# Kernel tuning notes

Hardware: AMD Instinct MI355X
Metric: run time of the kernel (lower is better)

Reference implementation:

```python
import jax, jax.numpy as jnp
import numpy as np

E, H, KVH, D = 2048, 16, 4, 128      # embed_dim, heads, kv heads, head_dim
HG, R, SYM, VAN = 12, 32, 4, 4       # graph heads, rel_rank, sym heads, vanilla heads
BASE = 10000
EPS = 1e-6


def _rms_norm(x, w):
    # RMSNorm over last dim (head_dim)
    return x * jax.lax.rsqrt(jnp.mean(x * x, axis=-1, keepdims=True) + EPS) * w


def _rotate_half(x):
    x1, x2 = jnp.split(x, 2, axis=-1)
    return jnp.concatenate([-x2, x1], axis=-1)


def _rope(q, k):
    # q, k: [B, H, S, D]
    S = q.shape[2]
    inv_freq = 1.0 / (BASE ** (jnp.arange(0, D, 2, dtype=jnp.float32) / D))
    t = jnp.arange(S, dtype=jnp.float32)
    freqs = jnp.outer(t, inv_freq)                       # [S, D/2]
    emb = jnp.concatenate([freqs, freqs], axis=-1)       # [S, D]
    cos = jnp.cos(emb)[None, None].astype(q.dtype)
    sin = jnp.sin(emb)[None, None].astype(q.dtype)
    return q * cos + _rotate_half(q) * sin, k * cos + _rotate_half(k) * sin


def setup_inputs() -> dict:
    key = jax.random.key(0)
    ks = jax.random.split(key, 9)
    B, S = 1, 2048
    std = 0.02
    return {
        'x': jax.random.normal(ks[0], (B, S, E), jnp.float32),
        'Wq': jax.random.normal(ks[1], (E, E), jnp.float32) * std,
        'Wk': jax.random.normal(ks[2], (KVH * D, E), jnp.float32) * std,
        'Wv': jax.random.normal(ks[3], (KVH * D, E), jnp.float32) * std,
        'Wo': jax.random.normal(ks[4], (E, E), jnp.float32) * std,
        'q_norm_w': jnp.ones((D,), jnp.float32),
        'k_norm_w': jnp.ones((D,), jnp.float32),
        'Wrq': jax.random.normal(ks[5], (HG * R, E), jnp.float32) * 0.01,
        'Wrk': jax.random.normal(ks[6], (HG * R, E), jnp.float32) * 0.01,
        'graph_scale': jax.random.normal(ks[7], (HG,), jnp.float32) * 0.1,
    }


def reference(x, Wq, Wk, Wv, Wo, q_norm_w, k_norm_w, Wrq, Wrk, graph_scale):
    B, S, _ = x.shape
    # projections -> [B, heads, S, D]
    q = (x @ Wq.T).reshape(B, S, H, D).transpose(0, 2, 1, 3)
    k = (x @ Wk.T).reshape(B, S, KVH, D).transpose(0, 2, 1, 3)
    v = (x @ Wv.T).reshape(B, S, KVH, D).transpose(0, 2, 1, 3)
    # QK-norm then RoPE
    q = _rms_norm(q, q_norm_w)
    k = _rms_norm(k, k_norm_w)
    q, k = _rope(q, k)
    # GQA: repeat kv heads
    rep = H // KVH
    k = jnp.repeat(k, rep, axis=1)
    v = jnp.repeat(v, rep, axis=1)
    # low-rank graph bias: [B, HG, S, S]
    Rq = (x @ Wrq.T).reshape(B, S, HG, R).transpose(0, 2, 1, 3)
    Rk = (x @ Wrk.T).reshape(B, S, HG, R).transpose(0, 2, 1, 3)
    bias = jnp.einsum('bhsr,bhtr->bhst', Rq, Rk)
    sym = bias[:, :SYM]
    sym = (sym + sym.transpose(0, 1, 3, 2)) * 0.5
    bias = jnp.concatenate([sym, bias[:, SYM:]], axis=1)
    bias = bias * graph_scale[None, :, None, None]
    # vanilla heads (last VAN heads) get zero bias
    bias = jnp.concatenate([bias, jnp.zeros((B, VAN, S, S), bias.dtype)], axis=1)
    # attention with causal mask
    scale = 1.0 / np.sqrt(D).astype(np.float32)
    scores = jnp.einsum('bhsd,bhtd->bhst', q, k) * scale + bias
    causal = jnp.tril(jnp.ones((S, S), bool))
    scores = jnp.where(causal[None, None], scores, jnp.finfo(scores.dtype).min)
    attn = jax.nn.softmax(scores, axis=-1)
    out = jnp.einsum('bhst,bhtd->bhsd', attn, v)
    out = out.transpose(0, 2, 1, 3).reshape(B, S, E)
    return out @ Wo.T
```

## Files before the change

kernel.cpp:

```cpp
#include <hip/hip_runtime.h>
#include <hip/hip_bf16.h>

typedef __attribute__((ext_vector_type(8))) short short8;
typedef __attribute__((ext_vector_type(4))) float f32x4;

__device__ __forceinline__ f32x4 mfma16(short8 a, short8 b, f32x4 c) {
  return __builtin_amdgcn_mfma_f32_16x16x32_bf16(a, b, c, 0, 0, 0);
}

__device__ __forceinline__ void gload_lds16(const void* g, void* l) {
  __builtin_amdgcn_global_load_lds(
      (const __attribute__((address_space(1))) void*)g,
      (__attribute__((address_space(3))) void*)l, 16, 0, 0);
}

struct __align__(8) bh4 { __hip_bfloat16 a, b, c, d; };
struct CastSeg { const float* src; __hip_bfloat16* dst; int n4; };
struct CastArgs { CastSeg seg[7]; int tot4; };

__global__ __launch_bounds__(256) void cast_all(CastArgs a) {
  int i = blockIdx.x * 256 + threadIdx.x;
  const int stride = gridDim.x * 256;
  for (; i < a.tot4; i += stride) {
    int j = i, s = 0;
    while (j >= a.seg[s].n4) { j -= a.seg[s].n4; ++s; }
    float4 v = ((const float4*)a.seg[s].src)[j];
    bh4 o{__float2bfloat16(v.x), __float2bfloat16(v.y),
          __float2bfloat16(v.z), __float2bfloat16(v.w)};
    ((bh4*)a.seg[s].dst)[j] = o;
  }
}

__global__ __launch_bounds__(256) void gemm_bt(const __hip_bfloat16* __restrict__ A,
                                               const __hip_bfloat16* __restrict__ B,
                                               float* __restrict__ C,
                                               int N, int K) {
  __shared__ __align__(16) __hip_bfloat16 As[128][32];
  __shared__ __align__(16) __hip_bfloat16 Bs[128][32];

  const int tid = threadIdx.x;
  const int lane = tid & 63, wv = tid >> 6;
  const int wm = (wv >> 1) * 64, wn = (wv & 1) * 64;
  const int l15 = lane & 15, g = lane >> 4;
  const int mb = blockIdx.y * 128, nb = blockIdx.x * 128;

  const int srow = wv * 32 + (lane >> 2);
  const int scol = (lane & 3) * 8;
  const __hip_bfloat16* Ap = A + (size_t)(mb + srow) * K + scol;
  const __hip_bfloat16* Bp = B + (size_t)(nb + srow) * K + scol;
  __hip_bfloat16* lA0 = &As[wv * 32][0];
  __hip_bfloat16* lA1 = &As[wv * 32 + 16][0];
  __hip_bfloat16* lB0 = &Bs[wv * 32][0];
  __hip_bfloat16* lB1 = &Bs[wv * 32 + 16][0];

  const f32x4 zf = {0.f, 0.f, 0.f, 0.f};
  f32x4 acc[4][4];
#pragma unroll
  for (int m = 0; m < 4; ++m)
#pragma unroll
    for (int n = 0; n < 4; ++n) acc[m][n] = zf;

  for (int k0 = 0; k0 < K; k0 += 32) {
    __syncthreads();
    gload_lds16(Ap + k0, lA0);
    gload_lds16(Ap + (size_t)16 * K + k0, lA1);
    gload_lds16(Bp + k0, lB0);
    gload_lds16(Bp + (size_t)16 * K + k0, lB1);
    __syncthreads();
    short8 af[4], bf[4];
#pragma unroll
    for (int m = 0; m < 4; ++m) af[m] = *(const short8*)&As[wm + m * 16 + l15][g * 8];
#pragma unroll
    for (int n = 0; n < 4; ++n) bf[n] = *(const short8*)&Bs[wn + n * 16 + l15][g * 8];
#pragma unroll
    for (int m = 0; m < 4; ++m)
#pragma unroll
      for (int n = 0; n < 4; ++n) acc[m][n] = mfma16(af[m], bf[n], acc[m][n]);
  }

#pragma unroll
  for (int m = 0; m < 4; ++m)
#pragma unroll
    for (int n = 0; n < 4; ++n)
#pragma unroll
      for (int r = 0; r < 4; ++r)
        C[(size_t)(mb + wm + m * 16 + g * 4 + r) * N + (nb + wn + n * 16 + l15)] =
            acc[m][n][r];
}

__global__ __launch_bounds__(256) void postproc(const float* __restrict__ C1,
                                                const float* __restrict__ qw,
                                                const float* __restrict__ kw,
                                                __hip_bfloat16* __restrict__ qn,
                                                __hip_bfloat16* __restrict__ kn,
                                                __hip_bfloat16* __restrict__ vt,
                                                __hip_bfloat16* __restrict__ rq,
                                                __hip_bfloat16* __restrict__ rk) {
  constexpr int S = 2048;
  const int s = blockIdx.x;
  const int tid = threadIdx.x;
  const int lane = tid & 63;
  const int wv = tid >> 6;
  const float* row = C1 + (size_t)s * 3840;

  const float f = exp2f(-(float)lane * (13.287712379549449f / 64.0f));
  const float ang = (float)s * f;
  float sn, cs;
  sincosf(ang, &sn, &cs);

  for (int hr = wv; hr < 20; hr += 4) {
    const float* base;
    __hip_bfloat16* dst;
    const float* nw;
    float oscale;
    if (hr < 16) {
      base = row + hr * 128;
      dst = qn + ((size_t)hr * S + s) * 128;
      nw = qw;
      oscale = 0.08838834764831845f;
    } else {
      const int h4 = hr - 16;
      base = row + 2048 + h4 * 128;
      dst = kn + ((size_t)h4 * S + s) * 128;
      nw = kw;
      oscale = 1.0f;
    }
    const float x1 = base[lane], x2 = base[lane + 64];
    float ss = x1 * x1 + x2 * x2;
#pragma unroll
    for (int mk = 1; mk < 64; mk <<= 1) ss += __shfl_xor(ss, mk);
    const float rms = rsqrtf(ss * (1.0f / 128.0f) + 1e-6f);
    const float x1n = x1 * rms * nw[lane];
    const float x2n = x2 * rms * nw[lane + 64];
    dst[lane]      = __float2bfloat16((x1n * cs - x2n * sn) * oscale);
    dst[lane + 64] = __float2bfloat16((x2n * cs + x1n * sn) * oscale);
  }
  for (int i = tid; i < 512; i += 256) {
    const int h4 = i >> 7, d = i & 127;
    vt[((size_t)h4 * 128 + d) * S + s] = __float2bfloat16(row[2560 + i]);
  }
  for (int i = tid; i < 768; i += 256) {
    if (i < 384) {
      rq[((size_t)(i >> 5) * S + s) * 32 + (i & 31)] = __float2bfloat16(row[3072 + i]);
    } else {
      const int j = i - 384;
      rk[((size_t)(j >> 5) * S + s) * 32 + (j & 31)] = __float2bfloat16(row[3072 + i]);
    }
  }
}

__global__ __launch_bounds__(256) void attn_kernel(const __hip_bfloat16* __restrict__ qn,
                                                   const __hip_bfloat16* __restrict__ kn,
                                                   const __hip_bfloat16* __restrict__ vt,
                                                   const __hip_bfloat16* __restrict__ rq,
                                                   const __hip_bfloat16* __restrict__ rk,
                                                   const float* __restrict__ gsc,
                                                   __hip_bfloat16* __restrict__ ao) {
  constexpr int S = 2048;
  constexpr float L2E = 1.4426950408889634f;
  const int h = blockIdx.x & 15;
  const int qb = 31 - (blockIdx.x >> 4);
  const int tid = threadIdx.x;
  const int lane = tid & 63;
  const int wv = tid >> 6;
  const int qs = qb * 64 + wv * 16;
  const int l15 = lane & 15, g = lane >> 4;
  const int h4 = h >> 2;
  const bool has_bias = (h < 12);
  const bool symh = (h < 4);
  const float gs = has_bias ? gsc[h] : 0.0f;
  const f32x4 zf = {0.f, 0.f, 0.f, 0.f};

  __shared__ __align__(16) char KsRaw[2][16384];
  __shared__ __align__(16) char VsRaw[2][16384];
  __shared__ __align__(16) __hip_bfloat16 p_lds[4][16][72];

  const int sxk = ((tid >> 4) & 7) << 4;
  const int sxv = ((tid >> 3) & 7) << 4;
  const int k_wr = (tid * 16) ^ sxk;
  const int v_wr = (tid * 16) ^ sxv;
  const int kx = (l15 & 7) << 4;

  short8 qf[4];
  {
    const __hip_bfloat16* qrow = qn + ((size_t)h * S + qs + l15) * 128 + g * 8;
#pragma unroll
    for (int kc = 0; kc < 4; ++kc) qf[kc] = *(const short8*)(qrow + kc * 32);
  }
  short8 rqA = {}, rkA = {};
  if (has_bias) rqA = *(const short8*)(rq + ((size_t)h * S + qs + l15) * 32 + g * 8);
  if (symh)     rkA = *(const short8*)(rk + ((size_t)h * S + qs + l15) * 32 + g * 8);

  float l_r[4] = {0.f, 0.f, 0.f, 0.f};
  f32x4 acc[8];
#pragma unroll
  for (int fb = 0; fb < 8; ++fb) acc[fb] = zf;

  const int nt = qb + 1;

  short8 kreg[4], vreg[4];
#pragma unroll
  for (int c = 0; c < 4; ++c) {
    kreg[c] = *(const short8*)(kn + ((size_t)(h4 * S + c * 16 + (tid >> 4))) * 128 + (tid & 15) * 8);
    vreg[c] = *(const short8*)(vt + ((size_t)(h4 * 128 + c * 32 + (tid >> 3))) * S + (tid & 7) * 8);
  }
#pragma unroll
  for (int c = 0; c < 4; ++c) {
    *(short8*)(&KsRaw[0][c * 4096 + k_wr]) = kreg[c];
    *(short8*)(&VsRaw[0][c * 4096 + v_wr]) = vreg[c];
  }
  if (nt > 1) {
#pragma unroll
    for (int c = 0; c < 4; ++c) {
      kreg[c] = *(const short8*)(kn + ((size_t)(h4 * S + 64 + c * 16 + (tid >> 4))) * 128 + (tid & 15) * 8);
      vreg[c] = *(const short8*)(vt + ((size_t)(h4 * 128 + c * 32 + (tid >> 3))) * S + 64 + (tid & 7) * 8);
    }
  }
  short8 rkB[4], rqB[4];
  if (has_bias) {
#pragma unroll
    for (int tf = 0; tf < 4; ++tf)
      rkB[tf] = *(const short8*)(rk + ((size_t)h * S + tf * 16 + l15) * 32 + g * 8);
    if (symh) {
#pragma unroll
      for (int tf = 0; tf < 4; ++tf)
        rqB[tf] = *(const short8*)(rq + ((size_t)h * S + tf * 16 + l15) * 32 + g * 8);
    }
  }
  __syncthreads();

  for (int t = 0; t < nt; ++t) {
    const int tbase = t * 64;
    const char* ksb = &KsRaw[t & 1][0];
    const char* vsb = &VsRaw[t & 1][0];

    f32x4 bias4[4];
    if (has_bias) {
#pragma unroll
      for (int tf = 0; tf < 4; ++tf) bias4[tf] = mfma16(rqA, rkB[tf], zf);
      if (symh) {
#pragma unroll
        for (int tf = 0; tf < 4; ++tf) {
          f32x4 b2 = mfma16(rkA, rqB[tf], zf);
#pragma unroll
          for (int r = 0; r < 4; ++r) bias4[tf][r] = 0.5f * (bias4[tf][r] + b2[r]);
        }
      }
      if (t + 1 < nt) {
        const int tb2 = tbase + 64;
#pragma unroll
        for (int tf = 0; tf < 4; ++tf)
          rkB[tf] = *(const short8*)(rk + ((size_t)h * S + tb2 + tf * 16 + l15) * 32 + g * 8);
        if (symh) {
#pragma unroll
          for (int tf = 0; tf < 4; ++tf)
            rqB[tf] = *(const short8*)(rq + ((size_t)h * S + tb2 + tf * 16 + l15) * 32 + g * 8);
        }
      }
    }

    f32x4 sc[4];
#pragma unroll
    for (int tf = 0; tf < 4; ++tf) {
      f32x4 s4 = zf;
#pragma unroll
      for (int kc = 0; kc < 4; ++kc) {
        short8 kf = *(const short8*)(ksb + ((((tf * 16 + l15) << 8) + (kc << 6) + (g << 4)) ^ kx));
        s4 = mfma16(qf[kc], kf, s4);
      }
#pragma unroll
      for (int r = 0; r < 4; ++r) {
        float sv = s4[r];
        if (has_bias) sv += gs * bias4[tf][r];
        if (tbase + tf * 16 + l15 > qs + g * 4 + r) sv = -1e30f;
        sc[tf][r] = sv;
      }
    }

#pragma unroll
    for (int tf = 0; tf < 4; ++tf)
#pragma unroll
      for (int r = 0; r < 4; ++r) {
        const float p = exp2f(sc[tf][r] * L2E);
        sc[tf][r] = p;
        l_r[r] += p;
      }

#pragma unroll
    for (int tf = 0; tf < 4; ++tf)
#pragma unroll
      for (int r = 0; r < 4; ++r)
        p_lds[wv][g * 4 + r][tf * 16 + l15] = __float2bfloat16(sc[tf][r]);
    const short8 pa0 = *(const short8*)((const char*)&p_lds[wv][l15][0] + g * 16);
    const short8 pa1 = *(const short8*)((const char*)&p_lds[wv][l15][32] + g * 16);

#pragma unroll
    for (int fb = 0; fb < 8; ++fb) {
      short8 v0 = *(const short8*)(vsb + ((((fb * 16 + l15) << 7) + (g << 4)) ^ kx));
      short8 v1 = *(const short8*)(vsb + ((((fb * 16 + l15) << 7) + 64 + (g << 4)) ^ kx));
      acc[fb] = mfma16(pa0, v0, acc[fb]);
      acc[fb] = mfma16(pa1, v1, acc[fb]);
    }

    if (t + 1 < nt) {
      char* ksw = &KsRaw[(t + 1) & 1][0];
      char* vsw = &VsRaw[(t + 1) & 1][0];
#pragma unroll
      for (int c = 0; c < 4; ++c) {
        *(short8*)(ksw + c * 4096 + k_wr) = kreg[c];
        *(short8*)(vsw + c * 4096 + v_wr) = vreg[c];
      }
      if (t + 2 < nt) {
        const int tb3 = tbase + 128;
#pragma unroll
        for (int c = 0; c < 4; ++c) {
          kreg[c] = *(const short8*)(kn + ((size_t)(h4 * S + tb3 + c * 16 + (tid >> 4))) * 128 + (tid & 15) * 8);
          vreg[c] = *(const short8*)(vt + ((size_t)(h4 * 128 + c * 32 + (tid >> 3))) * S + tb3 + (tid & 7) * 8);
        }
      }
      __syncthreads();
    }
  }

#pragma unroll
  for (int r = 0; r < 4; ++r) {
    float lv = l_r[r];
    lv += __shfl_xor(lv, 1);
    lv += __shfl_xor(lv, 2);
    lv += __shfl_xor(lv, 4);
    lv += __shfl_xor(lv, 8);
    l_r[r] = lv;
  }

#pragma unroll
  for (int fb = 0; fb < 8; ++fb)
#pragma unroll
    for (int r = 0; r < 4; ++r) {
      const int srow = qs + g * 4 + r;
      ao[(size_t)srow * 2048 + h * 128 + fb * 16 + l15] =
          __float2bfloat16(acc[fb][r] / l_r[r]);
    }
}

extern "C" void kernel_launch(void* const* d_in, const int* in_sizes, int n_in,
                              void* d_out, int out_size, void* d_ws, size_t ws_size,
                              hipStream_t stream) {
  (void)in_sizes; (void)n_in; (void)out_size; (void)ws_size;
  constexpr int S = 2048, E = 2048;

  const float* x   = (const float*)d_in[0];
  const float* Wq  = (const float*)d_in[1];
  const float* Wk  = (const float*)d_in[2];
  const float* Wv  = (const float*)d_in[3];
  const float* Wo  = (const float*)d_in[4];
  const float* qw  = (const float*)d_in[5];
  const float* kw  = (const float*)d_in[6];
  const float* Wrq = (const float*)d_in[7];
  const float* Wrk = (const float*)d_in[8];
  const float* gsc = (const float*)d_in[9];
  float* out = (float*)d_out;

  char* ws = (char*)d_ws;
  size_t off = 0;
  auto alloc = [&](size_t bytes) -> void* {
    void* p = ws + off;
    off += (bytes + 255) & ~(size_t)255;
    return p;
  };
  __hip_bfloat16* xb   = (__hip_bfloat16*)alloc((size_t)S * E * 2);
  __hip_bfloat16* Wall = (__hip_bfloat16*)alloc((size_t)3840 * E * 2);
  __hip_bfloat16* Wob  = (__hip_bfloat16*)alloc((size_t)E * E * 2);
  __hip_bfloat16* qnb  = (__hip_bfloat16*)alloc((size_t)16 * S * 128 * 2);
  __hip_bfloat16* knb  = (__hip_bfloat16*)alloc((size_t)4 * S * 128 * 2);
  __hip_bfloat16* vtb  = (__hip_bfloat16*)alloc((size_t)4 * 128 * S * 2);
  __hip_bfloat16* rqb  = (__hip_bfloat16*)alloc((size_t)12 * S * 32 * 2);
  __hip_bfloat16* rkb  = (__hip_bfloat16*)alloc((size_t)12 * S * 32 * 2);
  float* C1            = (float*)alloc((size_t)S * 3840 * 4);
  __hip_bfloat16* ao   = (__hip_bfloat16*)C1;

  CastArgs ca;
  ca.seg[0] = {x,   xb,                      (int)((size_t)S * E / 4)};
  ca.seg[1] = {Wq,  Wall,                    (int)((size_t)E * E / 4)};
  ca.seg[2] = {Wk,  Wall + (size_t)2048 * E, (int)((size_t)512 * E / 4)};
  ca.seg[3] = {Wv,  Wall + (size_t)2560 * E, (int)((size_t)512 * E / 4)};
  ca.seg[4] = {Wrq, Wall + (size_t)3072 * E, (int)((size_t)384 * E / 4)};
  ca.seg[5] = {Wrk, Wall + (size_t)3456 * E, (int)((size_t)384 * E / 4)};
  ca.seg[6] = {Wo,  Wob,                     (int)((size_t)E * E / 4)};
  ca.tot4 = 0;
  for (int i = 0; i < 7; ++i) ca.tot4 += ca.seg[i].n4;
  cast_all<<<dim3(2048), dim3(256), 0, stream>>>(ca);

  gemm_bt<<<dim3(30, 16), dim3(256), 0, stream>>>(xb, Wall, C1, 3840, E);
  postproc<<<dim3(2048), dim3(256), 0, stream>>>(C1, qw, kw, qnb, knb, vtb, rqb, rkb);
  attn_kernel<<<dim3(512), dim3(256), 0, stream>>>(qnb, knb, vtb, rqb, rkb, gsc, ao);
  gemm_bt<<<dim3(16, 16), dim3(256), 0, stream>>>(ao, Wob, out, E, E);
}
```

Measured before the change: 309.5 us.

## Split causal attention across key chunks with partial-result combine kernel

Each query block's key range is split into chunks of up to 8 tiles, raising the attention grid from 512 to 1280 blocks to even out causal load imbalance. Partial outputs are normalized per split and written with their row sums to scratch workspace, and a new combine kernel merges them with weighted sums. The P matrix transpose is also moved from LDS round-trips to lane shuffles by swapping MFMA operand order, and K/V staging drops to a single LDS buffer with an occupancy hint of 3. The cost is an extra kernel launch, scratch traffic for the partial outputs, and an extra barrier per tile from single buffering.

```diff
diff --git a/kernel.cpp b/kernel.cpp
--- a/kernel.cpp
+++ b/kernel.cpp
@@ -3,6 +3,7 @@
 
 typedef __attribute__((ext_vector_type(8))) short short8;
 typedef __attribute__((ext_vector_type(4))) float f32x4;
+typedef __attribute__((ext_vector_type(4))) unsigned int u32x4;
 
 __device__ __forceinline__ f32x4 mfma16(short8 a, short8 b, f32x4 c) {
   return __builtin_amdgcn_mfma_f32_16x16x32_bf16(a, b, c, 0, 0, 0);
@@ -12,6 +13,21 @@
   __builtin_amdgcn_global_load_lds(
       (const __attribute__((address_space(1))) void*)g,
       (__attribute__((address_space(3))) void*)l, 16, 0, 0);
+}
+
+__device__ __forceinline__ unsigned int bfp(float lo, float hi) {
+  return (unsigned int)__builtin_bit_cast(unsigned short, __float2bfloat16(lo)) |
+         ((unsigned int)__builtin_bit_cast(unsigned short, __float2bfloat16(hi)) << 16);
+}
+
+__device__ __forceinline__ float b2f(short s) {
+  return __builtin_bit_cast(float, ((unsigned int)(unsigned short)s) << 16);
+}
+
+__device__ __forceinline__ int qoff(int qb) {
+  if (qb < 16) return 2 * (qb - 8);
+  if (qb < 24) return 16 + 3 * (qb - 16);
+  return 40 + 4 * (qb - 24);
 }
 
 struct __align__(8) bh4 { __hip_bfloat16 a, b, c, d; };
@@ -149,17 +165,23 @@
   }
 }
 
-__global__ __launch_bounds__(256) void attn_kernel(const __hip_bfloat16* __restrict__ qn,
-                                                   const __hip_bfloat16* __restrict__ kn,
-                                                   const __hip_bfloat16* __restrict__ vt,
-                                                   const __hip_bfloat16* __restrict__ rq,
-                                                   const __hip_bfloat16* __restrict__ rk,
-                                                   const float* __restrict__ gsc,
-                                                   __hip_bfloat16* __restrict__ ao) {
+__global__ __launch_bounds__(256, 3) void attn_kernel(
+    const __hip_bfloat16* __restrict__ qn, const __hip_bfloat16* __restrict__ kn,
+    const __hip_bfloat16* __restrict__ vt, const __hip_bfloat16* __restrict__ rq,
+    const __hip_bfloat16* __restrict__ rk, const float* __restrict__ gsc,
+    __hip_bfloat16* __restrict__ ao, __hip_bfloat16* __restrict__ pO,
+    float* __restrict__ pL) {
   constexpr int S = 2048;
   constexpr float L2E = 1.4426950408889634f;
-  const int h = blockIdx.x & 15;
-  const int qb = 31 - (blockIdx.x >> 4);
+  const int bid = blockIdx.x;
+  const int h = bid & 15;
+  const int u = bid >> 4;
+  int qb, sp;
+  if (u < 32)      { qb = 31 - (u >> 2); sp = u & 3; }
+  else if (u < 56) { int v = u - 32; qb = 23 - v / 3; sp = v % 3; }
+  else if (u < 72) { int v = u - 56; qb = 15 - (v >> 1); sp = v & 1; }
+  else             { qb = 7 - (u - 72); sp = 0; }
+
   const int tid = threadIdx.x;
   const int lane = tid & 63;
   const int wv = tid >> 6;
@@ -171,9 +193,12 @@
   const float gs = has_bias ? gsc[h] : 0.0f;
   const f32x4 zf = {0.f, 0.f, 0.f, 0.f};
 
-  __shared__ __align__(16) char KsRaw[2][16384];
-  __shared__ __align__(16) char VsRaw[2][16384];
-  __shared__ __align__(16) __hip_bfloat16 p_lds[4][16][72];
+  const int nt = qb + 1;
+  const int t0 = sp * 8;
+  const int t1 = (t0 + 8 < nt) ? t0 + 8 : nt;
+
+  __shared__ __align__(16) char KsRaw[16384];
+  __shared__ __align__(16) char VsRaw[16384];
 
   const int sxk = ((tid >> 4) & 7) << 4;
   const int sxv = ((tid >> 3) & 7) << 4;
@@ -191,62 +216,63 @@
   if (has_bias) rqA = *(const short8*)(rq + ((size_t)h * S + qs + l15) * 32 + g * 8);
   if (symh)     rkA = *(const short8*)(rk + ((size_t)h * S + qs + l15) * 32 + g * 8);
 
-  float l_r[4] = {0.f, 0.f, 0.f, 0.f};
+  float lp = 0.0f;
   f32x4 acc[8];
 #pragma unroll
   for (int fb = 0; fb < 8; ++fb) acc[fb] = zf;
 
-  const int nt = qb + 1;
-
   short8 kreg[4], vreg[4];
 #pragma unroll
   for (int c = 0; c < 4; ++c) {
-    kreg[c] = *(const short8*)(kn + ((size_t)(h4 * S + c * 16 + (tid >> 4))) * 128 + (tid & 15) * 8);
-    vreg[c] = *(const short8*)(vt + ((size_t)(h4 * 128 + c * 32 + (tid >> 3))) * S + (tid & 7) * 8);
-  }
-#pragma unroll
-  for (int c = 0; c < 4; ++c) {
-    *(short8*)(&KsRaw[0][c * 4096 + k_wr]) = kreg[c];
-    *(short8*)(&VsRaw[0][c * 4096 + v_wr]) = vreg[c];
-  }
-  if (nt > 1) {
-#pragma unroll
-    for (int c = 0; c < 4; ++c) {
-      kreg[c] = *(const short8*)(kn + ((size_t)(h4 * S + 64 + c * 16 + (tid >> 4))) * 128 + (tid & 15) * 8);
-      vreg[c] = *(const short8*)(vt + ((size_t)(h4 * 128 + c * 32 + (tid >> 3))) * S + 64 + (tid & 7) * 8);
-    }
+    kreg[c] = *(const short8*)(kn + ((size_t)(h4 * S + t0 * 64 + c * 16 + (tid >> 4))) * 128 + (tid & 15) * 8);
+    vreg[c] = *(const short8*)(vt + ((size_t)(h4 * 128 + c * 32 + (tid >> 3))) * S + t0 * 64 + (tid & 7) * 8);
   }
   short8 rkB[4], rqB[4];
   if (has_bias) {
 #pragma unroll
     for (int tf = 0; tf < 4; ++tf)
-      rkB[tf] = *(const short8*)(rk + ((size_t)h * S + tf * 16 + l15) * 32 + g * 8);
+      rkB[tf] = *(const short8*)(rk + ((size_t)h * S + t0 * 64 + tf * 16 + l15) * 32 + g * 8);
     if (symh) {
 #pragma unroll
       for (int tf = 0; tf < 4; ++tf)
-        rqB[tf] = *(const short8*)(rq + ((size_t)h * S + tf * 16 + l15) * 32 + g * 8);
-    }
-  }
-  __syncthreads();
-
-  for (int t = 0; t < nt; ++t) {
+        rqB[tf] = *(const short8*)(rq + ((size_t)h * S + t0 * 64 + tf * 16 + l15) * 32 + g * 8);
+    }
+  }
+
+  const int srcA = l15 + ((g & 1) << 5);
+  const int srcB = srcA + 16;
+  const bool ghi = (g >= 2);
+
+  for (int t = t0; t < t1; ++t) {
     const int tbase = t * 64;
-    const char* ksb = &KsRaw[t & 1][0];
-    const char* vsb = &VsRaw[t & 1][0];
+#pragma unroll
+    for (int c = 0; c < 4; ++c) {
+      *(short8*)(&KsRaw[c * 4096 + k_wr]) = kreg[c];
+      *(short8*)(&VsRaw[c * 4096 + v_wr]) = vreg[c];
+    }
+    if (t + 1 < t1) {
+      const int tb2 = tbase + 64;
+#pragma unroll
+      for (int c = 0; c < 4; ++c) {
+        kreg[c] = *(const short8*)(kn + ((size_t)(h4 * S + tb2 + c * 16 + (tid >> 4))) * 128 + (tid & 15) * 8);
+        vreg[c] = *(const short8*)(vt + ((size_t)(h4 * 128 + c * 32 + (tid >> 3))) * S + tb2 + (tid & 7) * 8);
+      }
+    }
+    __syncthreads();
 
     f32x4 bias4[4];
     if (has_bias) {
 #pragma unroll
-      for (int tf = 0; tf < 4; ++tf) bias4[tf] = mfma16(rqA, rkB[tf], zf);
+      for (int tf = 0; tf < 4; ++tf) bias4[tf] = mfma16(rkB[tf], rqA, zf);
       if (symh) {
 #pragma unroll
         for (int tf = 0; tf < 4; ++tf) {
-          f32x4 b2 = mfma16(rkA, rqB[tf], zf);
+          f32x4 b2 = mfma16(rqB[tf], rkA, zf);
 #pragma unroll
           for (int r = 0; r < 4; ++r) bias4[tf][r] = 0.5f * (bias4[tf][r] + b2[r]);
         }
       }
-      if (t + 1 < nt) {
+      if (t + 1 < t1) {
         const int tb2 = tbase + 64;
 #pragma unroll
         for (int tf = 0; tf < 4; ++tf)
@@ -265,81 +291,121 @@
       f32x4 s4 = zf;
 #pragma unroll
       for (int kc = 0; kc < 4; ++kc) {
-        short8 kf = *(const short8*)(ksb + ((((tf * 16 + l15) << 8) + (kc << 6) + (g << 4)) ^ kx));
-        s4 = mfma16(qf[kc], kf, s4);
+        short8 kf = *(const short8*)(&KsRaw[((((tf * 16 + l15) << 8) + (kc << 6) + (g << 4)) ^ kx)]);
+        s4 = mfma16(kf, qf[kc], s4);
       }
 #pragma unroll
       for (int r = 0; r < 4; ++r) {
         float sv = s4[r];
         if (has_bias) sv += gs * bias4[tf][r];
-        if (tbase + tf * 16 + l15 > qs + g * 4 + r) sv = -1e30f;
-        sc[tf][r] = sv;
-      }
-    }
-
-#pragma unroll
-    for (int tf = 0; tf < 4; ++tf)
-#pragma unroll
-      for (int r = 0; r < 4; ++r) {
-        const float p = exp2f(sc[tf][r] * L2E);
+        if (tbase + tf * 16 + g * 4 + r > qs + l15) sv = -1e30f;
+        const float p = exp2f(sv * L2E);
+        lp += p;
         sc[tf][r] = p;
-        l_r[r] += p;
-      }
-
-#pragma unroll
-    for (int tf = 0; tf < 4; ++tf)
-#pragma unroll
-      for (int r = 0; r < 4; ++r)
-        p_lds[wv][g * 4 + r][tf * 16 + l15] = __float2bfloat16(sc[tf][r]);
-    const short8 pa0 = *(const short8*)((const char*)&p_lds[wv][l15][0] + g * 16);
-    const short8 pa1 = *(const short8*)((const char*)&p_lds[wv][l15][32] + g * 16);
+      }
+    }
+
+    unsigned int pk0[4], pk1[4];
+#pragma unroll
+    for (int tf = 0; tf < 4; ++tf) {
+      pk0[tf] = bfp(sc[tf][0], sc[tf][1]);
+      pk1[tf] = bfp(sc[tf][2], sc[tf][3]);
+    }
+    unsigned int a0[4], a1[4], b0[4], b1[4];
+#pragma unroll
+    for (int tf = 0; tf < 4; ++tf) {
+      a0[tf] = __shfl(pk0[tf], srcA);
+      a1[tf] = __shfl(pk1[tf], srcA);
+      b0[tf] = __shfl(pk0[tf], srcB);
+      b1[tf] = __shfl(pk1[tf], srcB);
+    }
+    u32x4 w0 = {ghi ? a0[1] : a0[0], ghi ? a1[1] : a1[0],
+                ghi ? b0[1] : b0[0], ghi ? b1[1] : b1[0]};
+    u32x4 w1 = {ghi ? a0[3] : a0[2], ghi ? a1[3] : a1[2],
+                ghi ? b0[3] : b0[2], ghi ? b1[3] : b1[2]};
+    const short8 pa0 = __builtin_bit_cast(short8, w0);
+    const short8 pa1 = __builtin_bit_cast(short8, w1);
 
 #pragma unroll
     for (int fb = 0; fb < 8; ++fb) {
-      short8 v0 = *(const short8*)(vsb + ((((fb * 16 + l15) << 7) + (g << 4)) ^ kx));
-      short8 v1 = *(const short8*)(vsb + ((((fb * 16 + l15) << 7) + 64 + (g << 4)) ^ kx));
+      short8 v0 = *(const short8*)(&VsRaw[((((fb * 16 + l15) << 7) + (g << 4)) ^ kx)]);
+      short8 v1 = *(const short8*)(&VsRaw[((((fb * 16 + l15) << 7) + 64 + (g << 4)) ^ kx)]);
       acc[fb] = mfma16(pa0, v0, acc[fb]);
       acc[fb] = mfma16(pa1, v1, acc[fb]);
     }
-
-    if (t + 1 < nt) {
-      char* ksw = &KsRaw[(t + 1) & 1][0];
-      char* vsw = &VsRaw[(t + 1) & 1][0];
-#pragma unroll
-      for (int c = 0; c < 4; ++c) {
-        *(short8*)(ksw + c * 4096 + k_wr) = kreg[c];
-        *(short8*)(vsw + c * 4096 + v_wr) = vreg[c];
-      }
-      if (t + 2 < nt) {
-        const int tb3 = tbase + 128;
-#pragma unroll
-        for (int c = 0; c < 4; ++c) {
-          kreg[c] = *(const short8*)(kn + ((size_t)(h4 * S + tb3 + c * 16 + (tid >> 4))) * 128 + (tid & 15) * 8);
-          vreg[c] = *(const short8*)(vt + ((size_t)(h4 * 128 + c * 32 + (tid >> 3))) * S + tb3 + (tid & 7) * 8);
-        }
-      }
-      __syncthreads();
-    }
-  }
-
-#pragma unroll
-  for (int r = 0; r < 4; ++r) {
-    float lv = l_r[r];
-    lv += __shfl_xor(lv, 1);
-    lv += __shfl_xor(lv, 2);
-    lv += __shfl_xor(lv, 4);
-    lv += __shfl_xor(lv, 8);
-    l_r[r] = lv;
-  }
-
-#pragma unroll
-  for (int fb = 0; fb < 8; ++fb)
-#pragma unroll
-    for (int r = 0; r < 4; ++r) {
-      const int srow = qs + g * 4 + r;
-      ao[(size_t)srow * 2048 + h * 128 + fb * 16 + l15] =
-          __float2bfloat16(acc[fb][r] / l_r[r]);
-    }
+    __syncthreads();
+  }
+
+  float lt = lp;
+  lt += __shfl_xor(lt, 16);
+  lt += __shfl_xor(lt, 32);
+  const float linv = 1.0f / lt;
+  float lr[4];
+#pragma unroll
+  for (int r = 0; r < 4; ++r) lr[r] = __shfl(linv, g * 4 + r);
+
+  if (qb <= 7) {
+#pragma unroll
+    for (int fb = 0; fb < 8; ++fb)
+#pragma unroll
+      for (int r = 0; r < 4; ++r) {
+        const int srow = qs + g * 4 + r;
+        ao[(size_t)srow * 2048 + h * 128 + fb * 16 + l15] =
+            __float2bfloat16(acc[fb][r] * lr[r]);
+      }
+  } else {
+    const int slot = h * 72 + qoff(qb) + sp;
+#pragma unroll
+    for (int fb = 0; fb < 8; ++fb)
+#pragma unroll
+      for (int r = 0; r < 4; ++r) {
+        pO[(size_t)slot * 8192 + (wv * 16 + g * 4 + r) * 128 + fb * 16 + l15] =
+            __float2bfloat16(acc[fb][r] * lr[r]);
+      }
+    if (g == 0) pL[slot * 64 + wv * 16 + l15] = lt;
+  }
+}
+
+__global__ __launch_bounds__(256) void attn_combine(const __hip_bfloat16* __restrict__ pO,
+                                                    const float* __restrict__ pL,
+                                                    __hip_bfloat16* __restrict__ ao) {
+  const int idx = blockIdx.x;
+  const int h = idx & 15;
+  const int qb = 8 + (idx >> 4);
+  const int nsplit = (qb + 8) >> 3;
+  const int slot0 = h * 72 + qoff(qb);
+  const int tid = threadIdx.x;
+
+  __shared__ float Lw[4][64];
+  __shared__ float Li[64];
+  if (tid < 64) {
+    float tot = 0.0f;
+    for (int s = 0; s < nsplit; ++s) {
+      const float w = pL[(slot0 + s) * 64 + tid];
+      Lw[s][tid] = w;
+      tot += w;
+    }
+    Li[tid] = 1.0f / tot;
+  }
+  __syncthreads();
+
+  for (int j = tid; j < 1024; j += 256) {
+    const int row = j >> 4;
+    const int cv = (j & 15) * 8;
+    float s8[8] = {0, 0, 0, 0, 0, 0, 0, 0};
+    for (int s = 0; s < nsplit; ++s) {
+      const short8 o = *(const short8*)(pO + (size_t)(slot0 + s) * 8192 + row * 128 + cv);
+      const float w = Lw[s][row];
+#pragma unroll
+      for (int e = 0; e < 8; ++e) s8[e] += w * b2f(o[e]);
+    }
+    const float inv = Li[row];
+    short8 ov;
+#pragma unroll
+    for (int e = 0; e < 8; ++e)
+      ov[e] = (short)__builtin_bit_cast(unsigned short, __float2bfloat16(s8[e] * inv));
+    *(short8*)(ao + (size_t)(qb * 64 + row) * 2048 + h * 128 + cv) = ov;
+  }
 }
 
 extern "C" void kernel_launch(void* const* d_in, const int* in_sizes, int n_in,
@@ -378,6 +444,9 @@
   float* C1            = (float*)alloc((size_t)S * 3840 * 4);
   __hip_bfloat16* ao   = (__hip_bfloat16*)C1;
 
+  __hip_bfloat16* pO = (__hip_bfloat16*)ws;
+  float* pL = (float*)(ws + 18874368);
+
   CastArgs ca;
   ca.seg[0] = {x,   xb,                      (int)((size_t)S * E / 4)};
   ca.seg[1] = {Wq,  Wall,                    (int)((size_t)E * E / 4)};
@@ -392,6 +461,8 @@
 
   gemm_bt<<<dim3(30, 16), dim3(256), 0, stream>>>(xb, Wall, C1, 3840, E);
   postproc<<<dim3(2048), dim3(256), 0, stream>>>(C1, qw, kw, qnb, knb, vtb, rqb, rkb);
-  attn_kernel<<<dim3(512), dim3(256), 0, stream>>>(qnb, knb, vtb, rqb, rkb, gsc, ao);
+  attn_kernel<<<dim3(1280), dim3(256), 0, stream>>>(qnb, knb, vtb, rqb, rkb, gsc,
+                                                    ao, pO, pL);
+  attn_combine<<<dim3(384), dim3(256), 0, stream>>>(pO, pL, ao);
   gemm_bt<<<dim3(16, 16), dim3(256), 0, stream>>>(ao, Wob, out, E, E);
 }
```

After: 450.4 us. 1.46x slower.
